# Performance work log

Hardware: AMD Instinct MI355X
Metric: run time of the kernel (lower is better)

Reference implementation:

```python
import jax, jax.numpy as jnp
from jax import lax
import numpy as np

LN_EPS = 1e-5


def _lstm_layer(x, w_ih, w_hh):
    """Single-layer LSTM, bias=False, batch_first. x: [B,T,I] -> hs: [B,T,H].
    PyTorch gate order: i, f, g, o along the 4H axis."""
    B, T, _ = x.shape
    H = w_hh.shape[1]
    # Precompute input projections for all timesteps in one GEMM: [B,T,4H]
    xg = jnp.einsum('bti,gi->btg', x, w_ih)

    def step(carry, xg_t):
        h, c = carry
        gates = xg_t + h @ w_hh.T  # [B,4H]
        i, f, g, o = jnp.split(gates, 4, axis=-1)
        c = jax.nn.sigmoid(f) * c + jax.nn.sigmoid(i) * jnp.tanh(g)
        h = jax.nn.sigmoid(o) * jnp.tanh(c)
        return (h, c), h

    init = (jnp.zeros((B, H), x.dtype), jnp.zeros((B, H), x.dtype))
    _, hs = lax.scan(step, init, jnp.swapaxes(xg, 0, 1))  # hs: [T,B,H]
    return jnp.swapaxes(hs, 0, 1)


def setup_inputs() -> dict:
    key = jax.random.key(0)
    ks = jax.random.split(key, 6)
    B, T, I, H, O = 256, 512, 1, 512, 1
    s_ih0 = 1.0 / np.sqrt(H)
    return {
        'input_seq': jax.random.normal(ks[0], (B, T, I), dtype=jnp.float32),
        'w_ih_l0': jax.random.normal(ks[1], (4 * H, I), dtype=jnp.float32) * s_ih0,
        'w_hh_l0': jax.random.normal(ks[2], (4 * H, H), dtype=jnp.float32) * s_ih0,
        'w_ih_l1': jax.random.normal(ks[3], (4 * H, H), dtype=jnp.float32) * s_ih0,
        'w_hh_l1': jax.random.normal(ks[4], (4 * H, H), dtype=jnp.float32) * s_ih0,
        'ln_gamma': jnp.ones((H,), dtype=jnp.float32),
        'ln_beta': jnp.zeros((H,), dtype=jnp.float32),
        'w_out': jax.random.normal(ks[5], (O, H), dtype=jnp.float32) * s_ih0,
    }


def reference(input_seq, w_ih_l0, w_hh_l0, w_ih_l1, w_hh_l1, ln_gamma, ln_beta, w_out):
    h1 = _lstm_layer(input_seq, w_ih_l0, w_hh_l0)  # [B,T,H]
    h2 = _lstm_layer(h1, w_ih_l1, w_hh_l1)         # [B,T,H]
    # Dropout is identity at inference. Only the last timestep is used downstream;
    # LayerNorm is per-position, so normalizing only h2[:, -1] matches the original.
    last = h2[:, -1, :]                             # [B,H]
    mu = jnp.mean(last, axis=-1, keepdims=True)
    var = jnp.mean(jnp.square(last - mu), axis=-1, keepdims=True)
    normed = (last - mu) * lax.rsqrt(var + LN_EPS) * ln_gamma + ln_beta
    return normed @ w_out.T                         # [B,1]
```

## Files before the change

### kernel.cpp

```cpp
#include <hip/hip_runtime.h>
#include <stdint.h>

#define BB 256
#define TT 512
#define HH 512
#define NBLK 256
#define SSTR 16
#define BBHH (BB*HH)

typedef __bf16 bf16x8 __attribute__((ext_vector_type(8)));
typedef float f32x4 __attribute__((ext_vector_type(4)));
typedef unsigned int u32x2 __attribute__((ext_vector_type(2)));

static __device__ __forceinline__ unsigned short f2bf(float f) {
    unsigned int u = __builtin_bit_cast(unsigned int, f);
    return (unsigned short)((u + 0x7fffu + ((u >> 16) & 1u)) >> 16);
}
static __device__ __forceinline__ bf16x8 packbf8(const float* p) {
    float4 a = *reinterpret_cast<const float4*>(p);
    float4 b = *reinterpret_cast<const float4*>(p + 4);
    unsigned short us[8] = { f2bf(a.x), f2bf(a.y), f2bf(a.z), f2bf(a.w),
                             f2bf(b.x), f2bf(b.y), f2bf(b.z), f2bf(b.w) };
    uint4 u; __builtin_memcpy(&u, us, 16);
    return __builtin_bit_cast(bf16x8, u);
}
static __device__ __forceinline__ float sigm(float x){ return 1.0f/(1.0f+__expf(-x)); }
static __device__ __forceinline__ float tanh_fast(float x){ return 2.0f/(1.0f+__expf(-2.0f*x)) - 1.0f; }

static __device__ __forceinline__ void ld_sys(uint4& d, const void* p) {
    asm volatile("global_load_dwordx4 %0, %1, off sc0 sc1" : "=v"(d) : "v"(p));
}
static __device__ __forceinline__ void st_sys2(void* p, u32x2 v) {
    asm volatile("global_store_dwordx2 %0, %1, off sc0 sc1" :: "v"(p), "v"(v) : "memory");
}
#define WAITVM(N) asm volatile("s_waitcnt vmcnt(" #N ")" ::: "memory")
#define SBAR      __builtin_amdgcn_sched_barrier(0)

__global__ __launch_bounds__(256) void prep_zero(unsigned short* __restrict__ h1p,
                                                 unsigned short* __restrict__ h2p,
                                                 int* __restrict__ slots) {
    int i = blockIdx.x * blockDim.x + threadIdx.x;
    for (int k = i; k < BBHH; k += gridDim.x * blockDim.x) { h1p[k] = 0; h2p[k] = 0; }
    if (i < NBLK * SSTR) slots[i] = 0;
}

__global__ __launch_bounds__(256, 1) void lstm_persist(
    const float* __restrict__ x,
    const float* __restrict__ wih0,
    const float* __restrict__ Whh0,
    const float* __restrict__ Wih1,
    const float* __restrict__ Whh1,
    unsigned short* __restrict__ h1buf,
    unsigned short* __restrict__ h2buf,
    int* __restrict__ slots)
{
    __shared__ float xf[16384];

    const int tid = threadIdx.x;
    const int w   = tid >> 6;
    const int l   = tid & 63;
    const int ln  = l & 15;
    const int kq  = l >> 4;
    const int bid = blockIdx.x;
    const bool isL0 = bid < 128;

    int g, cs, k0, mm = 0;
    const float* Wsrc;
    if (isL0) {
        g = bid >> 4; cs = bid & 15;
        k0 = w * 128;
        Wsrc = Whh0;
    } else {
        const int q = bid - 128;
        g = q >> 4; cs = q & 15;
        mm = w >> 1;
        k0 = (w & 1) * 256;
        Wsrc = mm ? Whh1 : Wih1;
    }

    bf16x8 wb[2][8][4];
    if (isL0) {
        #pragma unroll
        for (int nt = 0; nt < 2; ++nt)
            #pragma unroll
            for (int kb = 0; kb < 4; ++kb)
                #pragma unroll
                for (int g4 = 0; g4 < 4; ++g4)
                    wb[nt][kb][g4] = packbf8(Wsrc + (size_t)(g4 * HH + cs * 32 + nt * 16 + ln) * HH + k0 + kb * 32 + kq * 8);
    } else {
        #pragma unroll
        for (int nt = 0; nt < 2; ++nt)
            #pragma unroll
            for (int kb = 0; kb < 8; ++kb)
                #pragma unroll
                for (int g4 = 0; g4 < 4; ++g4)
                    wb[nt][kb][g4] = packbf8(Wsrc + (size_t)(g4 * HH + cs * 32 + nt * 16 + ln) * HH + k0 + kb * 32 + kq * 8);
    }

    const int erow = g * 32 + w * 8 + (l >> 3);
    f32x4 wiv[4] = {};
    if (isL0) {
        #pragma unroll
        for (int j = 0; j < 4; ++j) {
            const int cg = cs * 32 + (l & 7) * 4 + j;
            wiv[j] = (f32x4){ wih0[cg], wih0[512 + cg], wih0[1024 + cg], wih0[1536 + cg] };
        }
    }
    const int rt_r = w >> 1;
    const int rowl = (w & 1) * 8 + (l >> 3);
    const int nt_r = (l >> 2) & 1;
    const int colb = (l & 3) * 4;

    float cst[4] = {0.f, 0.f, 0.f, 0.f};

    for (int s = 0; s <= TT; ++s) {
        const bool active = isL0 ? (s < TT) : (s >= 1);
        if (active) {
            const int t = isL0 ? s : s - 1;
            const unsigned short* hp;
            if (isL0)    hp = h1buf + ((t - 1) & 1) * BBHH;
            else if (mm) hp = h2buf + ((t - 1) & 1) * BBHH;
            else         hp = h1buf + (t & 1) * BBHH;

            float xv = 0.f;
            if (isL0) xv = x[(size_t)erow * TT + t];

            f32x4 acc[2][2][4];
            #pragma unroll
            for (int rt = 0; rt < 2; ++rt)
                #pragma unroll
                for (int nt = 0; nt < 2; ++nt)
                    #pragma unroll
                    for (int g4 = 0; g4 < 4; ++g4) acc[rt][nt][g4] = (f32x4){0.f,0.f,0.f,0.f};

            const char* ab = (const char*)(hp + (size_t)(g * 32 + ln) * HH + k0 + kq * 8);
            uint4 A[4][2];
            #pragma unroll
            for (int kb = 0; kb < 4; ++kb) {
                ld_sys(A[kb][0], ab + kb * 64);
                ld_sys(A[kb][1], ab + 16384 + kb * 64);
            }

            #define MK(kb, ap) do { \
                _Pragma("unroll") \
                for (int rt = 0; rt < 2; ++rt) { \
                    bf16x8 av = __builtin_bit_cast(bf16x8, A[ap][rt]); \
                    _Pragma("unroll") \
                    for (int nt = 0; nt < 2; ++nt) \
                        _Pragma("unroll") \
                        for (int g4 = 0; g4 < 4; ++g4) \
                            acc[rt][nt][g4] = __builtin_amdgcn_mfma_f32_16x16x32_bf16(av, wb[nt][kb][g4], acc[rt][nt][g4], 0, 0, 0); \
                } } while (0)

            if (isL0) {
                WAITVM(6); SBAR; MK(0, 0);
                WAITVM(4); SBAR; MK(1, 1);
                WAITVM(2); SBAR; MK(2, 2);
                WAITVM(0); SBAR; MK(3, 3);
            } else {
                WAITVM(6); SBAR; MK(0, 0);
                ld_sys(A[0][0], ab + 256); ld_sys(A[0][1], ab + 16384 + 256);
                WAITVM(6); SBAR; MK(1, 1);
                ld_sys(A[1][0], ab + 320); ld_sys(A[1][1], ab + 16384 + 320);
                WAITVM(6); SBAR; MK(2, 2);
                ld_sys(A[2][0], ab + 384); ld_sys(A[2][1], ab + 16384 + 384);
                WAITVM(6); SBAR; MK(3, 3);
                ld_sys(A[3][0], ab + 448); ld_sys(A[3][1], ab + 16384 + 448);
                WAITVM(6); SBAR; MK(4, 0);
                WAITVM(4); SBAR; MK(5, 1);
                WAITVM(2); SBAR; MK(6, 2);
                WAITVM(0); SBAR; MK(7, 3);
            }
            #undef MK

            #pragma unroll
            for (int rt = 0; rt < 2; ++rt)
                #pragma unroll
                for (int nt = 0; nt < 2; ++nt)
                    #pragma unroll
                    for (int r = 0; r < 4; ++r) {
                        const int row16 = kq * 4 + r;
                        f32x4 v = { acc[rt][nt][0][r], acc[rt][nt][1][r],
                                    acc[rt][nt][2][r], acc[rt][nt][3][r] };
                        *(f32x4*)((char*)xf + (((w * 2 + rt) * 2 + nt) * 16 + row16) * 256
                                            + ((ln * 16) ^ ((row16 & 7) << 4))) = v;
                    }
            __syncthreads();

            unsigned short* ho = (isL0 ? h1buf : h2buf) + (t & 1) * BBHH;
            unsigned short hout[4];
            #pragma unroll
            for (int j = 0; j < 4; ++j) {
                f32x4 sv = (f32x4){0.f, 0.f, 0.f, 0.f};
                #pragma unroll
                for (int s4 = 0; s4 < 4; ++s4)
                    sv += *(const f32x4*)((const char*)xf + (((s4 * 2 + rt_r) * 2 + nt_r) * 16 + rowl) * 256
                                                          + (((colb + j) * 16) ^ ((rowl & 7) << 4)));
                if (isL0) sv += wiv[j] * xv;
                const float c = sigm(sv.y) * cst[j] + sigm(sv.x) * tanh_fast(sv.z);
                cst[j] = c;
                hout[j] = f2bf(sigm(sv.w) * tanh_fast(c));
            }
            u32x2 hv;
            hv.x = (unsigned int)hout[0] | ((unsigned int)hout[1] << 16);
            hv.y = (unsigned int)hout[2] | ((unsigned int)hout[3] << 16);
            st_sys2(ho + (size_t)erow * HH + cs * 32 + (l & 7) * 4, hv);
        }

        if (s < TT) {
            WAITVM(0);
            __syncthreads();
            if (tid == 0)
                __hip_atomic_store(slots + bid * SSTR, s + 1,
                                   __ATOMIC_RELAXED, __HIP_MEMORY_SCOPE_AGENT);
            if (tid < 32) {
                const int sid = (tid < 16) ? (g * 16 + tid) : (128 + g * 16 + (tid - 16));
                while (__hip_atomic_load(slots + sid * SSTR,
                                         __ATOMIC_RELAXED, __HIP_MEMORY_SCOPE_AGENT) < s + 1) {
                    __builtin_amdgcn_s_sleep(2);
                }
            }
            SBAR;
            __syncthreads();
        }
    }
}

__global__ __launch_bounds__(64) void ln_out_k(const unsigned short* __restrict__ h2,
                                               const float* __restrict__ gamma,
                                               const float* __restrict__ beta,
                                               const float* __restrict__ wout,
                                               float* __restrict__ out)
{
    const int row = blockIdx.x;
    const int lane = threadIdx.x;
    uint4 u = *reinterpret_cast<const uint4*>(h2 + row * HH + lane * 8);
    unsigned short us[8];
    *reinterpret_cast<uint4*>(us) = u;
    float v[8];
    #pragma unroll
    for (int j = 0; j < 8; ++j) {
        unsigned int ww = ((unsigned int)us[j]) << 16;
        v[j] = __builtin_bit_cast(float, ww);
    }
    float sum = 0.f;
    #pragma unroll
    for (int j = 0; j < 8; ++j) sum += v[j];
    #pragma unroll
    for (int o = 32; o >= 1; o >>= 1) sum += __shfl_xor(sum, o);
    const float mu = sum * (1.0f / 512.0f);

    float vs = 0.f;
    #pragma unroll
    for (int j = 0; j < 8; ++j) { float d = v[j] - mu; vs += d * d; }
    #pragma unroll
    for (int o = 32; o >= 1; o >>= 1) vs += __shfl_xor(vs, o);
    const float inv = rsqrtf(vs * (1.0f / 512.0f) + 1e-5f);

    float dot = 0.f;
    #pragma unroll
    for (int j = 0; j < 8; ++j) {
        const int c = lane * 8 + j;
        dot += ((v[j] - mu) * inv * gamma[c] + beta[c]) * wout[c];
    }
    #pragma unroll
    for (int o = 32; o >= 1; o >>= 1) dot += __shfl_xor(dot, o);
    if (lane == 0) out[row] = dot;
}

extern "C" void kernel_launch(void* const* d_in, const int* in_sizes, int n_in,
                              void* d_out, int out_size, void* d_ws, size_t ws_size,
                              hipStream_t stream) {
    const float* x     = (const float*)d_in[0];
    const float* wih0  = (const float*)d_in[1];
    const float* whh0  = (const float*)d_in[2];
    const float* wih1  = (const float*)d_in[3];
    const float* whh1  = (const float*)d_in[4];
    const float* gamma = (const float*)d_in[5];
    const float* beta  = (const float*)d_in[6];
    const float* wout  = (const float*)d_in[7];

    char* ws = (char*)d_ws;
    unsigned short* h1buf = (unsigned short*)(ws);
    unsigned short* h2buf = (unsigned short*)(ws + (512u << 10));
    int* slots            = (int*)(ws + (1024u << 10));

    hipLaunchKernelGGL(prep_zero, dim3(64), dim3(256), 0, stream,
                       h1buf + BBHH, h2buf + BBHH, slots);

    hipLaunchKernelGGL(lstm_persist, dim3(NBLK), dim3(256), 0, stream,
                       x, wih0, whh0, wih1, whh1, h1buf, h2buf, slots);

    hipLaunchKernelGGL(ln_out_k, dim3(BB), dim3(64), 0, stream,
                       h2buf + BBHH, gamma, beta, wout, (float*)d_out);
}
```

Before: 2.678 ms.

## Replace per-block flag barrier with per-group counters and deeper h1 buffering

Each group now signals progress through two shared counters that blocks bump with an atomic add, replacing per-block slots that 32 threads each polled. A single thread polls both counters. The h1 buffer grows to four slots so layer-0 blocks may run up to three steps ahead of layer 1, loosening the lockstep coupling between the layers. In exchange there is more counter contention and a larger workspace, and correctness now depends on the slack arithmetic matching the ring depth.

Result: slower. 3.083 ms (+15.1%).

```diff
diff --git a/kernel.cpp b/kernel.cpp
--- a/kernel.cpp
+++ b/kernel.cpp
@@ -5,7 +5,6 @@
 #define TT 512
 #define HH 512
 #define NBLK 256
-#define SSTR 16
 #define BBHH (BB*HH)
 
 typedef __bf16 bf16x8 __attribute__((ext_vector_type(8)));
@@ -36,12 +35,12 @@
 #define WAITVM(N) asm volatile("s_waitcnt vmcnt(" #N ")" ::: "memory")
 #define SBAR      __builtin_amdgcn_sched_barrier(0)
 
-__global__ __launch_bounds__(256) void prep_zero(unsigned short* __restrict__ h1p,
-                                                 unsigned short* __restrict__ h2p,
-                                                 int* __restrict__ slots) {
+__global__ __launch_bounds__(256) void prep_zero(unsigned short* __restrict__ h1p3,
+                                                 unsigned short* __restrict__ h2p1,
+                                                 int* __restrict__ cnt) {
     int i = blockIdx.x * blockDim.x + threadIdx.x;
-    for (int k = i; k < BBHH; k += gridDim.x * blockDim.x) { h1p[k] = 0; h2p[k] = 0; }
-    if (i < NBLK * SSTR) slots[i] = 0;
+    for (int k = i; k < BBHH; k += gridDim.x * blockDim.x) { h1p3[k] = 0; h2p1[k] = 0; }
+    if (i < 1024) cnt[i] = 0;
 }
 
 __global__ __launch_bounds__(256, 1) void lstm_persist(
@@ -52,7 +51,7 @@
     const float* __restrict__ Whh1,
     unsigned short* __restrict__ h1buf,
     unsigned short* __restrict__ h2buf,
-    int* __restrict__ slots)
+    int* __restrict__ cnt)
 {
     __shared__ float xf[16384];
 
@@ -111,6 +110,10 @@
     const int nt_r = (l >> 2) & 1;
     const int colb = (l & 3) * 4;
 
+    int* const mycnt = cnt + (g * 2 + (isL0 ? 0 : 1)) * 64;
+    const int* const c0p = cnt + g * 128;
+    const int* const c1p = cnt + g * 128 + 64;
+
     float cst[4] = {0.f, 0.f, 0.f, 0.f};
 
     for (int s = 0; s <= TT; ++s) {
@@ -118,9 +121,9 @@
         if (active) {
             const int t = isL0 ? s : s - 1;
             const unsigned short* hp;
-            if (isL0)    hp = h1buf + ((t - 1) & 1) * BBHH;
-            else if (mm) hp = h2buf + ((t - 1) & 1) * BBHH;
-            else         hp = h1buf + (t & 1) * BBHH;
+            if (isL0)    hp = h1buf + (size_t)((t - 1) & 3) * BBHH;
+            else if (mm) hp = h2buf + (size_t)((t - 1) & 1) * BBHH;
+            else         hp = h1buf + (size_t)(t & 3) * BBHH;
 
             float xv = 0.f;
             if (isL0) xv = x[(size_t)erow * TT + t];
@@ -187,7 +190,8 @@
                     }
             __syncthreads();
 
-            unsigned short* ho = (isL0 ? h1buf : h2buf) + (t & 1) * BBHH;
+            unsigned short* ho = isL0 ? (h1buf + (size_t)(t & 3) * BBHH)
+                                      : (h2buf + (size_t)(t & 1) * BBHH);
             unsigned short hout[4];
             #pragma unroll
             for (int j = 0; j < 4; ++j) {
@@ -207,21 +211,26 @@
             st_sys2(ho + (size_t)erow * HH + cs * 32 + (l & 7) * 4, hv);
         }
 
-        if (s < TT) {
-            WAITVM(0);
-            __syncthreads();
-            if (tid == 0)
-                __hip_atomic_store(slots + bid * SSTR, s + 1,
-                                   __ATOMIC_RELAXED, __HIP_MEMORY_SCOPE_AGENT);
-            if (tid < 32) {
-                const int sid = (tid < 16) ? (g * 16 + tid) : (128 + g * 16 + (tid - 16));
-                while (__hip_atomic_load(slots + sid * SSTR,
-                                         __ATOMIC_RELAXED, __HIP_MEMORY_SCOPE_AGENT) < s + 1) {
-                    __builtin_amdgcn_s_sleep(2);
+        WAITVM(0);
+        __syncthreads();
+        if (active && tid == 0)
+            __hip_atomic_fetch_add(mycnt, 1, __ATOMIC_RELAXED, __HIP_MEMORY_SCOPE_AGENT);
+
+        const int ns = s + 1;
+        if (ns <= TT) {
+            const bool nact = isL0 ? (ns < TT) : true;
+            if (nact) {
+                const int needL0 = 16 * ns;
+                const int needL1 = isL0 ? 16 * (ns - 3) : 16 * (ns - 1);
+                if (tid == 0) {
+                    while (__hip_atomic_load(c0p, __ATOMIC_RELAXED, __HIP_MEMORY_SCOPE_AGENT) < needL0 ||
+                           __hip_atomic_load(c1p, __ATOMIC_RELAXED, __HIP_MEMORY_SCOPE_AGENT) < needL1) {
+                        __builtin_amdgcn_s_sleep(1);
+                    }
                 }
+                SBAR;
+                __syncthreads();
             }
-            SBAR;
-            __syncthreads();
         }
     }
 }
@@ -282,14 +291,14 @@
 
     char* ws = (char*)d_ws;
     unsigned short* h1buf = (unsigned short*)(ws);
-    unsigned short* h2buf = (unsigned short*)(ws + (512u << 10));
-    int* slots            = (int*)(ws + (1024u << 10));
+    unsigned short* h2buf = (unsigned short*)(ws + (1024u << 10));
+    int* cnt              = (int*)(ws + (1536u << 10));
 
     hipLaunchKernelGGL(prep_zero, dim3(64), dim3(256), 0, stream,
-                       h1buf + BBHH, h2buf + BBHH, slots);
+                       h1buf + 3 * (size_t)BBHH, h2buf + BBHH, cnt);
 
     hipLaunchKernelGGL(lstm_persist, dim3(NBLK), dim3(256), 0, stream,
-                       x, wih0, whh0, wih1, whh1, h1buf, h2buf, slots);
+                       x, wih0, whh0, wih1, whh1, h1buf, h2buf, cnt);
 
     hipLaunchKernelGGL(ln_out_k, dim3(BB), dim3(64), 0, stream,
                        h2buf + BBHH, gamma, beta, wout, (float*)d_out);
```

## Decouple LSTM layer pipelines with quad-buffered h1 and per-layer step counters

Applied to the files above, without the earlier changes.

Replaces the global lockstep barrier between layer-0 and layer-1 blocks with asymmetric waits. Each layer now waits on its own peers for the current step and allows layer 0 to run up to three steps ahead of layer 1. To make that lag safe, the h1 buffer grows from double to quad buffering. This is meant to cut barrier stalls caused by skew between the two layers' block groups, at the cost of more workspace and more intricate slot semantics that could hide ordering bugs.

After: 2.738 ms. +2.2%, slower.

```diff
diff --git a/kernel.cpp b/kernel.cpp
--- a/kernel.cpp
+++ b/kernel.cpp
@@ -36,11 +36,11 @@
 #define WAITVM(N) asm volatile("s_waitcnt vmcnt(" #N ")" ::: "memory")
 #define SBAR      __builtin_amdgcn_sched_barrier(0)
 
-__global__ __launch_bounds__(256) void prep_zero(unsigned short* __restrict__ h1p,
-                                                 unsigned short* __restrict__ h2p,
+__global__ __launch_bounds__(256) void prep_zero(unsigned short* __restrict__ h1p3,
+                                                 unsigned short* __restrict__ h2p1,
                                                  int* __restrict__ slots) {
     int i = blockIdx.x * blockDim.x + threadIdx.x;
-    for (int k = i; k < BBHH; k += gridDim.x * blockDim.x) { h1p[k] = 0; h2p[k] = 0; }
+    for (int k = i; k < BBHH; k += gridDim.x * blockDim.x) { h1p3[k] = 0; h2p1[k] = 0; }
     if (i < NBLK * SSTR) slots[i] = 0;
 }
 
@@ -118,9 +118,9 @@
         if (active) {
             const int t = isL0 ? s : s - 1;
             const unsigned short* hp;
-            if (isL0)    hp = h1buf + ((t - 1) & 1) * BBHH;
-            else if (mm) hp = h2buf + ((t - 1) & 1) * BBHH;
-            else         hp = h1buf + (t & 1) * BBHH;
+            if (isL0)    hp = h1buf + (size_t)((t - 1) & 3) * BBHH;
+            else if (mm) hp = h2buf + (size_t)((t - 1) & 1) * BBHH;
+            else         hp = h1buf + (size_t)(t & 3) * BBHH;
 
             float xv = 0.f;
             if (isL0) xv = x[(size_t)erow * TT + t];
@@ -187,7 +187,8 @@
                     }
             __syncthreads();
 
-            unsigned short* ho = (isL0 ? h1buf : h2buf) + (t & 1) * BBHH;
+            unsigned short* ho = isL0 ? (h1buf + (size_t)(t & 3) * BBHH)
+                                      : (h2buf + (size_t)(t & 1) * BBHH);
             unsigned short hout[4];
             #pragma unroll
             for (int j = 0; j < 4; ++j) {
@@ -210,18 +211,28 @@
         if (s < TT) {
             WAITVM(0);
             __syncthreads();
-            if (tid == 0)
-                __hip_atomic_store(slots + bid * SSTR, s + 1,
+            if (active && tid == 0)
+                __hip_atomic_store(slots + bid * SSTR, isL0 ? s + 1 : s,
                                    __ATOMIC_RELAXED, __HIP_MEMORY_SCOPE_AGENT);
-            if (tid < 32) {
-                const int sid = (tid < 16) ? (g * 16 + tid) : (128 + g * 16 + (tid - 16));
-                while (__hip_atomic_load(slots + sid * SSTR,
-                                         __ATOMIC_RELAXED, __HIP_MEMORY_SCOPE_AGENT) < s + 1) {
-                    __builtin_amdgcn_s_sleep(2);
+            const int ns = s + 1;
+            const bool nextAct = isL0 ? (ns < TT) : true;
+            if (nextAct) {
+                if (tid < 32) {
+                    const int* sp;
+                    int thr;
+                    if (tid < 16) {
+                        sp  = slots + (g * 16 + tid) * SSTR;
+                        thr = ns;
+                    } else {
+                        sp  = slots + (128 + g * 16 + (tid - 16)) * SSTR;
+                        thr = isL0 ? ns - 3 : ns - 1;
+                    }
+                    while (__hip_atomic_load(sp, __ATOMIC_RELAXED, __HIP_MEMORY_SCOPE_AGENT) < thr)
+                        __builtin_amdgcn_s_sleep(2);
                 }
+                SBAR;
+                __syncthreads();
             }
-            SBAR;
-            __syncthreads();
         }
     }
 }
@@ -282,11 +293,11 @@
 
     char* ws = (char*)d_ws;
     unsigned short* h1buf = (unsigned short*)(ws);
-    unsigned short* h2buf = (unsigned short*)(ws + (512u << 10));
-    int* slots            = (int*)(ws + (1024u << 10));
+    unsigned short* h2buf = (unsigned short*)(ws + (1024u << 10));
+    int* slots            = (int*)(ws + (1536u << 10));
 
     hipLaunchKernelGGL(prep_zero, dim3(64), dim3(256), 0, stream,
-                       h1buf + BBHH, h2buf + BBHH, slots);
+                       h1buf + 3 * (size_t)BBHH, h2buf + BBHH, slots);
 
     hipLaunchKernelGGL(lstm_persist, dim3(NBLK), dim3(256), 0, stream,
                        x, wih0, whh0, wih1, whh1, h1buf, h2buf, slots);
```
